# Optimization experiments

Hardware: AMD Instinct MI355X
Metric: run time of the kernel (lower is better)

## Reference

```python
import jax, jax.numpy as jnp
import numpy as np

NUM_HEADS = 8
KEY_DIM = 32
ATTN_RATIO = 4
RESOLUTION = 7
VAL_DIM = KEY_DIM * ATTN_RATIO  # 128
SCALE = KEY_DIM ** (-0.5)


def _bias_idxs():
    # (2, N) grid positions, N = resolution^2
    r = RESOLUTION
    gh, gw = np.meshgrid(np.arange(r), np.arange(r), indexing='ij')
    pos = np.stack([gh, gw], 0).reshape(2, -1)
    rel = np.abs(pos[:, :, None] - pos[:, None, :])
    return jnp.asarray(rel[0] * r + rel[1], dtype=jnp.int32)  # (N, N)


def setup_inputs() -> dict:
    key = jax.random.key(0)
    ks = jax.random.split(key, 4)
    B, N, D = 2048, RESOLUTION * RESOLUTION, 384
    qkv_out = KEY_DIM * NUM_HEADS * 2 + VAL_DIM * NUM_HEADS  # 1536
    return {
        'x': jax.random.normal(ks[0], (B, N, D), jnp.float32),
        'qkv_kernel': jax.random.normal(ks[1], (D, qkv_out), jnp.float32) * 0.02,
        'qkv_bias': jnp.zeros((qkv_out,), jnp.float32),
        'proj_kernel': jax.random.normal(ks[2], (VAL_DIM * NUM_HEADS, D), jnp.float32) * 0.02,
        'proj_bias': jnp.zeros((D,), jnp.float32),
        'attention_biases': jax.random.normal(ks[3], (NUM_HEADS, N), jnp.float32) * 0.02,
    }


def reference(x, qkv_kernel, qkv_bias, proj_kernel, proj_bias, attention_biases):
    B, N, _ = x.shape
    idxs = _bias_idxs()  # (N, N) int32
    qkv = jnp.matmul(x, qkv_kernel) + qkv_bias            # (B, N, 1536)
    qkv = qkv.reshape(B, N, NUM_HEADS, -1).transpose(0, 2, 1, 3)  # (B, H, N, 2k+v)
    q = qkv[..., :KEY_DIM]
    k = qkv[..., KEY_DIM:2 * KEY_DIM]
    v = qkv[..., 2 * KEY_DIM:]
    attn = jnp.einsum('bhnd,bhmd->bhnm', q, k) * SCALE    # (B, H, N, N)
    bias = attention_biases[:, idxs]                       # (H, N, N) gather
    attn = jax.nn.softmax(attn + bias, axis=-1)
    out = jnp.einsum('bhnm,bhmd->bhnd', attn, v)           # (B, H, N, val_dim)
    out = out.transpose(0, 2, 1, 3).reshape(B, N, NUM_HEADS * VAL_DIM)
    return jnp.matmul(out, proj_kernel) + proj_bias
```

## Files before the change

### kernel.cpp

```cpp
#include <hip/hip_runtime.h>
#include <hip/hip_bf16.h>

using bf16x8 = short __attribute__((ext_vector_type(8)));
using f32x16 = float __attribute__((ext_vector_type(16)));

#define MROWS 100352
#define SCALE_Q 0.17677669529663687f

static __device__ __forceinline__ unsigned short f2bs(float f){
  unsigned u = __builtin_bit_cast(unsigned, f);
  unsigned r = (u + 0x7FFFu + ((u >> 16) & 1u)) >> 16;
  return (unsigned short)r;
}
static __device__ __forceinline__ unsigned packbf(float a, float b){
  return (unsigned)f2bs(a) | ((unsigned)f2bs(b) << 16);
}

__global__ void k_convert(const float* __restrict__ qkvW, const float* __restrict__ qkvB,
                          const float* __restrict__ projW, const float* __restrict__ ab,
                          short* __restrict__ WqkvT, short* __restrict__ WpT,
                          float* __restrict__ bqkv, float* __restrict__ bias_exp){
  int i = blockIdx.x*256 + threadIdx.x;
  if (i < 1536*384){
    int c = i/384, f = i - c*384;
    int src; float sc = 1.0f;
    if (c < 512){ src = (c>>6)*192 + (c&63); if ((c&63) < 32) sc = SCALE_Q; }
    else        { int dv = c - 512; src = (dv>>7)*192 + 64 + (dv&127); }
    WqkvT[i] = (short)f2bs(qkvW[f*1536 + src] * sc);
    return;
  }
  i -= 1536*384;
  if (i < 384*1024){
    int j = i/1024, m = i - j*1024;
    WpT[i] = (short)f2bs(projW[m*384 + j]);
    return;
  }
  i -= 384*1024;
  if (i < 1536){
    int c = i; int src; float sc = 1.0f;
    if (c < 512){ src = (c>>6)*192 + (c&63); if ((c&63) < 32) sc = SCALE_Q; }
    else        { int dv = c - 512; src = (dv>>7)*192 + 64 + (dv&127); }
    bqkv[c] = qkvB[src] * sc;
    return;
  }
  i -= 1536;
  if (i < 8*64*49){
    int h = i / (64*49), rem = i - h*(64*49);
    int r = rem / 49, n = rem - r*49;
    float v = 0.0f;
    if (r < 49){
      int rh = r/7, rw = r - rh*7, ch = n/7, cw = n - ch*7;
      int dh = rh>ch?rh-ch:ch-rh, dw = rw>cw?rw-cw:cw-rw;
      v = ab[h*49 + dh*7 + dw];
    }
    bias_exp[i] = v;
  }
}

__global__ __launch_bounds__(512) void k_qkv3(const float* __restrict__ x,
                                              const short* __restrict__ WqkvT,
                                              const float* __restrict__ bqkv,
                                              short* __restrict__ qkvbuf){
  __shared__ short Alds[128*64];
  __shared__ short Blds[256*64];
  const int lane = threadIdx.x & 63, w = threadIdx.x >> 6;
  const int hi = lane >> 5, l31 = lane & 31;
  const int wm = w >> 2, wn = w & 3;

  const int nwg = 6*784;
  const int lin = blockIdx.x + 6*blockIdx.y;
  const int swz = (lin & 7)*(nwg>>3) + (lin>>3);
  const int slab = swz % 6, panel = swz / 6;
  const size_t R0 = (size_t)panel*128, C0 = (size_t)slab*256;

  const int rs = threadIdx.x >> 2;
  const int cb = threadIdx.x & 3;
  const float* xrow = x + (R0 + rs)*384 + cb*16;
  const int adr0 = rs*64 + (((2*cb)   ^ (rs&7))<<3);
  const int adr1 = rs*64 + (((2*cb+1) ^ (rs&7))<<3);

  const int srow = lane >> 3;
  const int sG   = ((lane & 7) ^ srow) * 8;
  const short* bG = WqkvT + (C0 + (size_t)(w*8 + srow))*384 + sG;

  {
    const float4 g0 = *reinterpret_cast<const float4*>(xrow);
    const float4 g1 = *reinterpret_cast<const float4*>(xrow+4);
    const float4 g2 = *reinterpret_cast<const float4*>(xrow+8);
    const float4 g3 = *reinterpret_cast<const float4*>(xrow+12);
    bf16x8 t0, t1;
    t0[0]=(short)f2bs(g0.x); t0[1]=(short)f2bs(g0.y); t0[2]=(short)f2bs(g0.z); t0[3]=(short)f2bs(g0.w);
    t0[4]=(short)f2bs(g1.x); t0[5]=(short)f2bs(g1.y); t0[6]=(short)f2bs(g1.z); t0[7]=(short)f2bs(g1.w);
    t1[0]=(short)f2bs(g2.x); t1[1]=(short)f2bs(g2.y); t1[2]=(short)f2bs(g2.z); t1[3]=(short)f2bs(g2.w);
    t1[4]=(short)f2bs(g3.x); t1[5]=(short)f2bs(g3.y); t1[6]=(short)f2bs(g3.z); t1[7]=(short)f2bs(g3.w);
    *reinterpret_cast<bf16x8*>(&Alds[adr0]) = t0;
    *reinterpret_cast<bf16x8*>(&Alds[adr1]) = t1;
    #pragma unroll
    for (int j=0; j<4; ++j)
      __builtin_amdgcn_global_load_lds(
        (const unsigned int __attribute__((address_space(1)))*)(bG + (size_t)j*64*384),
        (unsigned int __attribute__((address_space(3)))*)(&Blds[(j*64 + w*8)*64]), 16, 0, 0);
  }
  __syncthreads();

  f32x16 acc[2][2];
  acc[0][0]=(f32x16)0.f; acc[0][1]=(f32x16)0.f; acc[1][0]=(f32x16)0.f; acc[1][1]=(f32x16)0.f;

  for (int kt=0; kt<6; ++kt){
    float4 g0,g1,g2,g3;
    if (kt < 5){
      const float* p = xrow + (kt+1)*64;
      g0 = *reinterpret_cast<const float4*>(p);
      g1 = *reinterpret_cast<const float4*>(p+4);
      g2 = *reinterpret_cast<const float4*>(p+8);
      g3 = *reinterpret_cast<const float4*>(p+12);
    }
    #pragma unroll
    for (int ks=0; ks<4; ++ks){
      bf16x8 aF[2], bF[2];
      #pragma unroll
      for (int mt=0; mt<2; ++mt){
        const int rA = wm*64 + mt*32 + l31;
        aF[mt] = *reinterpret_cast<const bf16x8*>(
                   (const char*)Alds + rA*128 + ((((ks<<1)|hi) ^ (rA&7))<<4));
      }
      #pragma unroll
      for (int nt=0; nt<2; ++nt){
        const int rB = wn*64 + nt*32 + l31;
        bF[nt] = *reinterpret_cast<const bf16x8*>(
                   (const char*)Blds + rB*128 + ((((ks<<1)|hi) ^ (rB&7))<<4));
      }
      #pragma unroll
      for (int mt=0; mt<2; ++mt)
        #pragma unroll
        for (int nt=0; nt<2; ++nt)
          acc[mt][nt] = __builtin_amdgcn_mfma_f32_32x32x16_bf16(aF[mt], bF[nt], acc[mt][nt], 0,0,0);
    }
    __syncthreads();
    if (kt < 5){
      bf16x8 t0, t1;
      t0[0]=(short)f2bs(g0.x); t0[1]=(short)f2bs(g0.y); t0[2]=(short)f2bs(g0.z); t0[3]=(short)f2bs(g0.w);
      t0[4]=(short)f2bs(g1.x); t0[5]=(short)f2bs(g1.y); t0[6]=(short)f2bs(g1.z); t0[7]=(short)f2bs(g1.w);
      t1[0]=(short)f2bs(g2.x); t1[1]=(short)f2bs(g2.y); t1[2]=(short)f2bs(g2.z); t1[3]=(short)f2bs(g2.w);
      t1[4]=(short)f2bs(g3.x); t1[5]=(short)f2bs(g3.y); t1[6]=(short)f2bs(g3.z); t1[7]=(short)f2bs(g3.w);
      *reinterpret_cast<bf16x8*>(&Alds[adr0]) = t0;
      *reinterpret_cast<bf16x8*>(&Alds[adr1]) = t1;
      #pragma unroll
      for (int j=0; j<4; ++j)
        __builtin_amdgcn_global_load_lds(
          (const unsigned int __attribute__((address_space(1)))*)(bG + (size_t)j*64*384 + (kt+1)*64),
          (unsigned int __attribute__((address_space(3)))*)(&Blds[(j*64 + w*8)*64]), 16, 0, 0);
    }
    __syncthreads();
  }

  #pragma unroll
  for (int nt=0; nt<2; ++nt){
    const int c = (int)C0 + wn*64 + nt*32 + l31;
    const float bb = bqkv[c];
    #pragma unroll
    for (int mt=0; mt<2; ++mt){
      const size_t rbase = R0 + wm*64 + mt*32;
      #pragma unroll
      for (int rg=0; rg<16; ++rg){
        const size_t r = rbase + (rg&3) + 8*(rg>>2) + 4*hi;
        qkvbuf[r*1536 + c] = (short)f2bs(acc[mt][nt][rg] + bb);
      }
    }
  }
}

__global__ __launch_bounds__(256) void k_proj4(const short* __restrict__ A,
                                               const short* __restrict__ Bw,
                                               const float* __restrict__ bias,
                                               float* __restrict__ out){
  __shared__ short Alds[128*64];
  __shared__ short Blds[128*64];
  const int lane = threadIdx.x & 63, w = threadIdx.x >> 6;
  const int hi = lane >> 5, l31 = lane & 31;
  const int wm = w >> 1, wn = w & 1;

  const int nwg = 3 * 784;
  const int lin = blockIdx.x + 3 * blockIdx.y;
  const int swz = (lin & 7) * (nwg >> 3) + (lin >> 3);
  const int slab = swz % 3, panel = swz / 3;
  const size_t R0 = (size_t)panel * 128, C0 = (size_t)slab * 128;

  f32x16 acc[2][2];
  acc[0][0]=(f32x16)0.f; acc[0][1]=(f32x16)0.f; acc[1][0]=(f32x16)0.f; acc[1][1]=(f32x16)0.f;

  const int srow = lane >> 3;
  const int sG   = ((lane & 7) ^ srow) * 8;
  const short* aG = A  + (R0 + (size_t)(w*8 + srow))*1024 + sG;
  const short* bG = Bw + (C0 + (size_t)(w*8 + srow))*1024 + sG;

  for (int kt=0; kt<16; ++kt){
    #pragma unroll
    for (int j=0; j<4; ++j){
      __builtin_amdgcn_global_load_lds(
        (const unsigned int __attribute__((address_space(1)))*)(aG + (size_t)j*32*1024 + kt*64),
        (unsigned int __attribute__((address_space(3)))*)(&Alds[(j*32 + w*8)*64]), 16, 0, 0);
      __builtin_amdgcn_global_load_lds(
        (const unsigned int __attribute__((address_space(1)))*)(bG + (size_t)j*32*1024 + kt*64),
        (unsigned int __attribute__((address_space(3)))*)(&Blds[(j*32 + w*8)*64]), 16, 0, 0);
    }
    __syncthreads();
    #pragma unroll
    for (int ks=0; ks<4; ++ks){
      bf16x8 aF[2], bF[2];
      #pragma unroll
      for (int mt=0; mt<2; ++mt){
        const int rA = wm*64 + mt*32 + l31;
        aF[mt] = *reinterpret_cast<const bf16x8*>(
                   (const char*)Alds + rA*128 + ((((ks<<1)|hi) ^ (rA&7))<<4));
      }
      #pragma unroll
      for (int nt=0; nt<2; ++nt){
        const int rB = wn*64 + nt*32 + l31;
        bF[nt] = *reinterpret_cast<const bf16x8*>(
                   (const char*)Blds + rB*128 + ((((ks<<1)|hi) ^ (rB&7))<<4));
      }
      #pragma unroll
      for (int mt=0; mt<2; ++mt)
        #pragma unroll
        for (int nt=0; nt<2; ++nt)
          acc[mt][nt] = __builtin_amdgcn_mfma_f32_32x32x16_bf16(aF[mt], bF[nt], acc[mt][nt], 0,0,0);
    }
    __syncthreads();
  }

  #pragma unroll
  for (int nt=0; nt<2; ++nt){
    const int c = (int)C0 + wn*64 + nt*32 + l31;
    const float bb = bias[c];
    #pragma unroll
    for (int mt=0; mt<2; ++mt){
      const size_t rbase = R0 + wm*64 + mt*32;
      #pragma unroll
      for (int rg=0; rg<16; ++rg){
        const size_t r = rbase + (rg&3) + 8*(rg>>2) + 4*hi;
        out[r*384 + c] = acc[mt][nt][rg] + bb;
      }
    }
  }
}

__global__ __launch_bounds__(256) void k_attn(const short* __restrict__ qkvbuf,
                                              const float* __restrict__ bias_exp, short* __restrict__ aout){
  const int lane = threadIdx.x & 63, w = threadIdx.x >> 6;
  const int hi = lane >> 5, l31 = lane & 31;
  const int b = blockIdx.x, hg = blockIdx.y;
  const int h = hg*4 + w;

  __shared__ short vlds[4*49*136];

  for (int i=0; i<13; ++i){
    const int n = i*4 + w;
    if (n < 49){
      const bf16x8 vv = *reinterpret_cast<const bf16x8*>(qkvbuf + (b*49+n)*1536 + 512 + hg*512 + lane*8);
      const int hh = lane >> 4;
      const int d0 = ((lane & 15) * 8) ^ (((n>>3)&1) << 5);
      *reinterpret_cast<bf16x8*>(&vlds[(hh*49 + n)*136 + d0]) = vv;
    }
  }
  __syncthreads();

  bf16x8 kf[2][2];
  #pragma unroll
  for (int mt=0; mt<2; ++mt){
    const int n = 32*mt + l31;
    #pragma unroll
    for (int ks=0; ks<2; ++ks)
      kf[mt][ks] = (n < 49)
        ? *reinterpret_cast<const bf16x8*>(qkvbuf + (b*49+n)*1536 + h*64 + 32 + ks*16 + hi*8)
        : (bf16x8)(short)0;
  }
  const short* vb = &vlds[w*49*136];
  const int dxbase = hi << 5;

  for (int rb=0; rb<2; ++rb){
    const int r = 32*rb + l31;
    bf16x8 qf[2];
    #pragma unroll
    for (int ks=0; ks<2; ++ks)
      qf[ks] = (r < 49)
        ? *reinterpret_cast<const bf16x8*>(qkvbuf + (b*49+r)*1536 + h*64 + ks*16 + hi*8)
        : (bf16x8)(short)0;

    f32x16 s[2];
    s[0] = (f32x16)0.0f; s[1] = (f32x16)0.0f;
    #pragma unroll
    for (int ks=0; ks<2; ++ks){
      s[0] = __builtin_amdgcn_mfma_f32_32x32x16_bf16(kf[0][ks], qf[ks], s[0], 0, 0, 0);
      s[1] = __builtin_amdgcn_mfma_f32_32x32x16_bf16(kf[1][ks], qf[ks], s[1], 0, 0, 0);
    }

    float mloc = -3.0e38f;
    #pragma unroll
    for (int mt=0; mt<2; ++mt)
      #pragma unroll
      for (int rg=0; rg<16; ++rg){
        const int n = 32*mt + (rg&3) + 8*(rg>>2) + 4*hi;
        float v = s[mt][rg];
        v = (n < 49) ? v + bias_exp[(h*64 + r)*49 + n] : -1.0e30f;
        s[mt][rg] = v;
        mloc = fmaxf(mloc, v);
      }
    const float mrow = fmaxf(mloc, __shfl_xor(mloc, 32));
    float sloc = 0.0f;
    #pragma unroll
    for (int mt=0; mt<2; ++mt)
      #pragma unroll
      for (int rg=0; rg<16; ++rg){
        const float p = __expf(s[mt][rg] - mrow);
        s[mt][rg] = p; sloc += p;
      }
    const float inv = 1.0f / (sloc + __shfl_xor(sloc, 32));
    #pragma unroll
    for (int mt=0; mt<2; ++mt)
      #pragma unroll
      for (int rg=0; rg<16; ++rg) s[mt][rg] *= inv;

    unsigned pk[8][2];
    #pragma unroll
    for (int o=0; o<8; ++o){
      const int mt = o>>2, base = 4*(o&3);
      pk[o][0] = packbf(s[mt][base+0], s[mt][base+1]);
      pk[o][1] = packbf(s[mt][base+2], s[mt][base+3]);
    }
    bf16x8 af[4];
    #pragma unroll
    for (int ks=0; ks<4; ++ks){
      const unsigned e0 = pk[2*ks][0],   e1 = pk[2*ks][1];
      const unsigned o0 = pk[2*ks+1][0], o1 = pk[2*ks+1][1];
      const unsigned own0 = hi ? o0 : e0, own1 = hi ? o1 : e1;
      const unsigned oth0 = hi ? e0 : o0, oth1 = hi ? e1 : o1;
      const unsigned sw0 = __shfl_xor(oth0, 32), sw1 = __shfl_xor(oth1, 32);
      const unsigned lo0 = hi ? sw0 : own0, lo1 = hi ? sw1 : own1;
      const unsigned h0  = hi ? own0 : sw0, h1  = hi ? own1 : sw1;
      union { bf16x8 v; unsigned u[4]; } t;
      t.u[0]=lo0; t.u[1]=lo1; t.u[2]=h0; t.u[3]=h1;
      af[ks] = t.v;
    }

    #pragma unroll
    for (int dt=0; dt<4; ++dt){
      const int dx = (dt*32 + l31) ^ dxbase;
      f32x16 acc = (f32x16)0.0f;
      #pragma unroll
      for (int ks=0; ks<4; ++ks){
        bf16x8 t;
        if (ks < 3){
          const int nb = ks*16 + hi*8;
          #pragma unroll
          for (int j=0; j<8; ++j) t[j] = vb[(nb + j)*136 + dx];
        } else {
          #pragma unroll
          for (int j=0; j<8; ++j) t[j] = 0;
          if (hi == 0) t[0] = vb[48*136 + (dt*32 + l31)];
        }
        acc = __builtin_amdgcn_mfma_f32_32x32x16_bf16(af[ks], t, acc, 0, 0, 0);
      }
      #pragma unroll
      for (int rg=0; rg<16; ++rg){
        const int rr = 32*rb + (rg&3) + 8*(rg>>2) + 4*hi;
        if (rr < 49)
          aout[(b*49+rr)*1024 + h*128 + dt*32 + l31] = (short)f2bs(acc[rg]);
      }
    }
  }
}

extern "C" void kernel_launch(void* const* d_in, const int* in_sizes, int n_in,
                              void* d_out, int out_size, void* d_ws, size_t ws_size,
                              hipStream_t stream) {
  const float* x     = (const float*)d_in[0];
  const float* qkvW  = (const float*)d_in[1];
  const float* qkvB  = (const float*)d_in[2];
  const float* projW = (const float*)d_in[3];
  const float* projB = (const float*)d_in[4];
  const float* ab    = (const float*)d_in[5];

  char* ws = (char*)d_ws;
  short* aoutb = (short*)ws;
  size_t off = (size_t)MROWS*1024*2;
  short* qkvbuf = (short*)(ws + off); off += (size_t)MROWS*1536*2;
  short* WqkvT  = (short*)(ws + off); off += (size_t)1536*384*2;
  short* WpT    = (short*)(ws + off); off += (size_t)384*1024*2;
  float* bqkv   = (float*)(ws + off); off += (size_t)1536*4;
  float* bias_exp = (float*)(ws + off); off += (size_t)8*64*49*4;
  if (ws_size < off) return;

  const int conv_total = 1536*384 + 384*1024 + 1536 + 8*64*49;
  k_convert<<<(conv_total + 255)/256, 256, 0, stream>>>(qkvW, qkvB, projW, ab,
                                                        WqkvT, WpT, bqkv, bias_exp);
  k_qkv3<<<dim3(6, 784), 512, 0, stream>>>(x, WqkvT, bqkv, qkvbuf);
  k_attn<<<dim3(2048, 2), 256, 0, stream>>>(qkvbuf, bias_exp, aoutb);
  k_proj4<<<dim3(3, 784), 256, 0, stream>>>(aoutb, WpT, projB, (float*)d_out);
}
```

Before: 480.6 us.

## Double-buffer weight tiles and use 4 waves with larger per-wave tiles in QKV GEMM

The QKV projection kernel now runs 256 threads (4 waves) per block instead of 512, and each wave computes a 64x128 output tile with 8 accumulators. The weight tile in LDS is double-buffered, so the async global-to-LDS load for the next k-step is issued before the MFMA loop on the current one. The x tile is still single-buffered, staged through registers and fenced by barriers. The intent is to overlap weight loads with compute and cut barrier count, at the cost of more registers and LDS per block, which may lower occupancy.

```diff
diff --git a/kernel.cpp b/kernel.cpp
--- a/kernel.cpp
+++ b/kernel.cpp
@@ -57,15 +57,16 @@
   }
 }
 
-__global__ __launch_bounds__(512) void k_qkv3(const float* __restrict__ x,
+__global__ __launch_bounds__(256) void k_qkv4(const float* __restrict__ x,
                                               const short* __restrict__ WqkvT,
                                               const float* __restrict__ bqkv,
                                               short* __restrict__ qkvbuf){
   __shared__ short Alds[128*64];
-  __shared__ short Blds[256*64];
-  const int lane = threadIdx.x & 63, w = threadIdx.x >> 6;
+  __shared__ short Blds[2][256*64];
+  const int t = threadIdx.x;
+  const int lane = t & 63, w = t >> 6;
   const int hi = lane >> 5, l31 = lane & 31;
-  const int wm = w >> 2, wn = w & 3;
+  const int wm = w >> 1, wn = w & 1;
 
   const int nwg = 6*784;
   const int lin = blockIdx.x + 6*blockIdx.y;
@@ -73,51 +74,53 @@
   const int slab = swz % 6, panel = swz / 6;
   const size_t R0 = (size_t)panel*128, C0 = (size_t)slab*256;
 
-  const int rs = threadIdx.x >> 2;
-  const int cb = threadIdx.x & 3;
-  const float* xrow = x + (R0 + rs)*384 + cb*16;
-  const int adr0 = rs*64 + (((2*cb)   ^ (rs&7))<<3);
-  const int adr1 = rs*64 + (((2*cb+1) ^ (rs&7))<<3);
-
+  const int rs = t >> 1, hb = t & 1;
+  const float* xrow = x + (R0 + rs)*384 + hb*32;
   const int srow = lane >> 3;
-  const int sG   = ((lane & 7) ^ srow) * 8;
+  const int sG = ((lane & 7) ^ srow) * 8;
   const short* bG = WqkvT + (C0 + (size_t)(w*8 + srow))*384 + sG;
 
-  {
-    const float4 g0 = *reinterpret_cast<const float4*>(xrow);
-    const float4 g1 = *reinterpret_cast<const float4*>(xrow+4);
-    const float4 g2 = *reinterpret_cast<const float4*>(xrow+8);
-    const float4 g3 = *reinterpret_cast<const float4*>(xrow+12);
-    bf16x8 t0, t1;
-    t0[0]=(short)f2bs(g0.x); t0[1]=(short)f2bs(g0.y); t0[2]=(short)f2bs(g0.z); t0[3]=(short)f2bs(g0.w);
-    t0[4]=(short)f2bs(g1.x); t0[5]=(short)f2bs(g1.y); t0[6]=(short)f2bs(g1.z); t0[7]=(short)f2bs(g1.w);
-    t1[0]=(short)f2bs(g2.x); t1[1]=(short)f2bs(g2.y); t1[2]=(short)f2bs(g2.z); t1[3]=(short)f2bs(g2.w);
-    t1[4]=(short)f2bs(g3.x); t1[5]=(short)f2bs(g3.y); t1[6]=(short)f2bs(g3.z); t1[7]=(short)f2bs(g3.w);
-    *reinterpret_cast<bf16x8*>(&Alds[adr0]) = t0;
-    *reinterpret_cast<bf16x8*>(&Alds[adr1]) = t1;
-    #pragma unroll
-    for (int j=0; j<4; ++j)
-      __builtin_amdgcn_global_load_lds(
-        (const unsigned int __attribute__((address_space(1)))*)(bG + (size_t)j*64*384),
-        (unsigned int __attribute__((address_space(3)))*)(&Blds[(j*64 + w*8)*64]), 16, 0, 0);
-  }
+  float4 ar[8];
+
+  #pragma unroll
+  for (int i=0; i<8; ++i) ar[i] = *reinterpret_cast<const float4*>(xrow + i*4);
+  #pragma unroll
+  for (int i=0; i<4; ++i){
+    const float4 u0 = ar[2*i], u1 = ar[2*i+1];
+    bf16x8 tt;
+    tt[0]=(short)f2bs(u0.x); tt[1]=(short)f2bs(u0.y); tt[2]=(short)f2bs(u0.z); tt[3]=(short)f2bs(u0.w);
+    tt[4]=(short)f2bs(u1.x); tt[5]=(short)f2bs(u1.y); tt[6]=(short)f2bs(u1.z); tt[7]=(short)f2bs(u1.w);
+    const int clog = hb*4 + i;
+    *reinterpret_cast<bf16x8*>(&Alds[rs*64 + ((clog ^ (rs&7))<<3)]) = tt;
+  }
+  #pragma unroll
+  for (int j=0; j<8; ++j)
+    __builtin_amdgcn_global_load_lds(
+      (const unsigned int __attribute__((address_space(1)))*)(bG + (size_t)j*32*384),
+      (unsigned int __attribute__((address_space(3)))*)(&Blds[0][(j*32 + w*8)*64]), 16, 0, 0);
   __syncthreads();
 
-  f32x16 acc[2][2];
-  acc[0][0]=(f32x16)0.f; acc[0][1]=(f32x16)0.f; acc[1][0]=(f32x16)0.f; acc[1][1]=(f32x16)0.f;
+  f32x16 acc[2][4];
+  #pragma unroll
+  for (int mt=0; mt<2; ++mt)
+    #pragma unroll
+    for (int nt=0; nt<4; ++nt) acc[mt][nt] = (f32x16)0.0f;
 
   for (int kt=0; kt<6; ++kt){
-    float4 g0,g1,g2,g3;
+    const int cur = kt & 1;
     if (kt < 5){
-      const float* p = xrow + (kt+1)*64;
-      g0 = *reinterpret_cast<const float4*>(p);
-      g1 = *reinterpret_cast<const float4*>(p+4);
-      g2 = *reinterpret_cast<const float4*>(p+8);
-      g3 = *reinterpret_cast<const float4*>(p+12);
+      #pragma unroll
+      for (int j=0; j<8; ++j)
+        __builtin_amdgcn_global_load_lds(
+          (const unsigned int __attribute__((address_space(1)))*)(bG + (size_t)j*32*384 + (kt+1)*64),
+          (unsigned int __attribute__((address_space(3)))*)(&Blds[cur^1][(j*32 + w*8)*64]), 16, 0, 0);
+      #pragma unroll
+      for (int i=0; i<8; ++i)
+        ar[i] = *reinterpret_cast<const float4*>(xrow + (kt+1)*64 + i*4);
     }
     #pragma unroll
     for (int ks=0; ks<4; ++ks){
-      bf16x8 aF[2], bF[2];
+      bf16x8 aF[2], bF[4];
       #pragma unroll
       for (int mt=0; mt<2; ++mt){
         const int rA = wm*64 + mt*32 + l31;
@@ -125,38 +128,35 @@
                    (const char*)Alds + rA*128 + ((((ks<<1)|hi) ^ (rA&7))<<4));
       }
       #pragma unroll
-      for (int nt=0; nt<2; ++nt){
-        const int rB = wn*64 + nt*32 + l31;
+      for (int nt=0; nt<4; ++nt){
+        const int rB = wn*128 + nt*32 + l31;
         bF[nt] = *reinterpret_cast<const bf16x8*>(
-                   (const char*)Blds + rB*128 + ((((ks<<1)|hi) ^ (rB&7))<<4));
+                   (const char*)Blds[cur] + rB*128 + ((((ks<<1)|hi) ^ (rB&7))<<4));
       }
       #pragma unroll
       for (int mt=0; mt<2; ++mt)
         #pragma unroll
-        for (int nt=0; nt<2; ++nt)
+        for (int nt=0; nt<4; ++nt)
           acc[mt][nt] = __builtin_amdgcn_mfma_f32_32x32x16_bf16(aF[mt], bF[nt], acc[mt][nt], 0,0,0);
     }
-    __syncthreads();
     if (kt < 5){
-      bf16x8 t0, t1;
-      t0[0]=(short)f2bs(g0.x); t0[1]=(short)f2bs(g0.y); t0[2]=(short)f2bs(g0.z); t0[3]=(short)f2bs(g0.w);
-      t0[4]=(short)f2bs(g1.x); t0[5]=(short)f2bs(g1.y); t0[6]=(short)f2bs(g1.z); t0[7]=(short)f2bs(g1.w);
-      t1[0]=(short)f2bs(g2.x); t1[1]=(short)f2bs(g2.y); t1[2]=(short)f2bs(g2.z); t1[3]=(short)f2bs(g2.w);
-      t1[4]=(short)f2bs(g3.x); t1[5]=(short)f2bs(g3.y); t1[6]=(short)f2bs(g3.z); t1[7]=(short)f2bs(g3.w);
-      *reinterpret_cast<bf16x8*>(&Alds[adr0]) = t0;
-      *reinterpret_cast<bf16x8*>(&Alds[adr1]) = t1;
-      #pragma unroll
-      for (int j=0; j<4; ++j)
-        __builtin_amdgcn_global_load_lds(
-          (const unsigned int __attribute__((address_space(1)))*)(bG + (size_t)j*64*384 + (kt+1)*64),
-          (unsigned int __attribute__((address_space(3)))*)(&Blds[(j*64 + w*8)*64]), 16, 0, 0);
-    }
-    __syncthreads();
-  }
-
-  #pragma unroll
-  for (int nt=0; nt<2; ++nt){
-    const int c = (int)C0 + wn*64 + nt*32 + l31;
+      __syncthreads();
+      #pragma unroll
+      for (int i=0; i<4; ++i){
+        const float4 u0 = ar[2*i], u1 = ar[2*i+1];
+        bf16x8 tt;
+        tt[0]=(short)f2bs(u0.x); tt[1]=(short)f2bs(u0.y); tt[2]=(short)f2bs(u0.z); tt[3]=(short)f2bs(u0.w);
+        tt[4]=(short)f2bs(u1.x); tt[5]=(short)f2bs(u1.y); tt[6]=(short)f2bs(u1.z); tt[7]=(short)f2bs(u1.w);
+        const int clog = hb*4 + i;
+        *reinterpret_cast<bf16x8*>(&Alds[rs*64 + ((clog ^ (rs&7))<<3)]) = tt;
+      }
+      __syncthreads();
+    }
+  }
+
+  #pragma unroll
+  for (int nt=0; nt<4; ++nt){
+    const int c = (int)C0 + wn*128 + nt*32 + l31;
     const float bb = bqkv[c];
     #pragma unroll
     for (int mt=0; mt<2; ++mt){
@@ -394,7 +394,7 @@
   const int conv_total = 1536*384 + 384*1024 + 1536 + 8*64*49;
   k_convert<<<(conv_total + 255)/256, 256, 0, stream>>>(qkvW, qkvB, projW, ab,
                                                         WqkvT, WpT, bqkv, bias_exp);
-  k_qkv3<<<dim3(6, 784), 512, 0, stream>>>(x, WqkvT, bqkv, qkvbuf);
+  k_qkv4<<<dim3(6, 784), 256, 0, stream>>>(x, WqkvT, bqkv, qkvbuf);
   k_attn<<<dim3(2048, 2), 256, 0, stream>>>(qkvbuf, bias_exp, aoutb);
   k_proj4<<<dim3(3, 784), 256, 0, stream>>>(aoutb, WpT, projB, (float*)d_out);
 }
```

Result: slower. 521.1 us (+8.4%).
